# Performance work log

Measured on AMD Instinct MI355X. Metric: run time of the kernel, lower is better.

The kernel has to match this reference:

```python
import jax, jax.numpy as jnp
import numpy as np

DIM = 256
HALF = DIM // 2
B, S = 32, 4096
U_MAX = 4096          # upper bound on number of unique tree positions (positions < S)
MAX_DEPTH = 13        # bitlen(S) covers all path lengths for positions <= S


def setup_inputs() -> dict:
    key = jax.random.key(0)
    k1, k2, k3, k4, k5 = jax.random.split(key, 5)
    token_types = jax.random.randint(k1, (B, S), 0, 5, dtype=jnp.int32)
    node_positions = jax.random.randint(k2, (B, S), 0, S, dtype=jnp.int32)
    small_vals = jax.random.randint(k3, (B, S), 0, 4, dtype=jnp.int32)
    # deBruijn tokens (type 4) reference tree positions -> values must lie in unique(node_positions)
    token_values = jnp.where(token_types == 4, node_positions,
                   jnp.where(token_types == 3, -1, small_vals)).astype(jnp.int32)
    primitives = jax.random.normal(k4, (2, HALF, HALF), dtype=jnp.float32)
    identity = jnp.ones((1, HALF), dtype=jnp.float32)
    embed_weight = jax.random.normal(k5, (11, HALF), dtype=jnp.float32)
    return {"token_types": token_types, "token_values": token_values,
            "node_positions": node_positions, "primitives": primitives,
            "identity": identity, "embed_weight": embed_weight}


def cayley(X):
    # torch orthogonal(..., orthogonal_map='cayley'): A = tril(X) - tril(X)^T (skew), Q = (I - A/2)^{-1}(I + A/2)
    A = jnp.tril(X)
    A = A - jnp.swapaxes(A, -1, -2)
    I = jnp.eye(X.shape[-1], dtype=X.dtype)
    return jnp.linalg.solve(I - 0.5 * A, I + 0.5 * A)


def _forward(token_types, token_values, node_positions, primitives, identity, embed_weight):
    Q = cayley(primitives)                                   # [2, h, h] orthogonal maps
    flat_pos = node_positions.ravel()
    uniq, inv = jnp.unique(flat_pos, return_inverse=True, size=U_MAX, fill_value=S)
    inv = inv.ravel()

    # binary path of pos: bit d of pos for d < bitlen(pos)-1, padded with 2 (pos<=1 -> empty path)
    d = jnp.arange(MAX_DEPTH, dtype=uniq.dtype)
    bits = (uniq[:, None] >> d) & 1                           # [U, D]
    valid = (uniq[:, None] >> (d + 1)) > 0
    word = jnp.where(valid, bits, 2)                          # [U, D]

    maps0 = jnp.broadcast_to(identity, (U_MAX, HALF)).astype(primitives.dtype)

    def step(maps, b):                                        # maps [U, h], b [U]
        m0 = maps @ Q[0].T                                    # linear(maps, primitives[0])
        m1 = maps @ Q[1].T
        maps = jnp.where((b == 0)[:, None], m0,
                jnp.where((b == 1)[:, None], m1, maps))
        return maps, None

    path_emb, _ = jax.lax.scan(step, maps0, word.T)           # [U, h]

    pos_enc = path_emb[inv].reshape(B, S, HALF)               # positional encodings

    sos = token_types == 0
    bop = token_types == 1
    nop = token_types == 2
    oos = (token_types == 3) & (token_values == -1)
    db = token_types == 4

    emb_idx = jnp.where(bop, token_values + 1,
              jnp.where(nop, token_values + 5, 0))
    type_emb = embed_weight[emb_idx]                          # [B, S, h]

    db_idx = jnp.searchsorted(uniq, jnp.clip(token_values, 0, S - 1))  # bucketize into unique positions
    db_emb = path_emb[db_idx]                                 # [B, S, h]

    content = jnp.zeros_like(pos_enc)
    content = jnp.where(sos[..., None], embed_weight[0], content)
    content = jnp.where((bop | nop)[..., None], type_emb, content)
    content = jnp.where(db[..., None], db_emb, content)
    content = jnp.where(oos[..., None], embed_weight[10], content)

    return jnp.concatenate([content, pos_enc], axis=-1)       # [B, S, DIM]


def reference(token_types, token_values, node_positions, primitives, identity, embed_weight):
    return _forward(token_types, token_values, node_positions, primitives, identity, embed_weight)
```

## Files before the change

### kernel.cpp

```cpp
#include <hip/hip_runtime.h>

#define HALF 128
#define NMAT 16384
#define NTOK 131072

typedef float f4 __attribute__((ext_vector_type(4)));

__device__ __forceinline__ float nval(const float* __restrict__ X, int r, int c) {
    int mx = r > c ? r : c;
    int mn = r ^ c ^ mx;
    float x = X[mx * HALF + mn];
    return (r == c) ? 1.0f : (r > c ? 0.5f * x : -0.5f * x);
}

template<bool FIRST, bool LAST>
__global__ __launch_bounds__(256) void k1_step(const float* __restrict__ prim,
                                               const float* __restrict__ Win,
                                               float* __restrict__ Wout,
                                               int S) {
    __shared__ __align__(16) float Rs[16][132];
    __shared__ float Dc[16][17];
    __shared__ __align__(16) float RBs[16][132];
    __shared__ float Cs[16][17];

    const int blk = blockIdx.x;
    const int b   = blk >> 3;
    const int rg  = blk & 7;
    const int r0  = rg << 4;
    const int t   = threadIdx.x;
    const int k0  = S << 4;
    const float* __restrict__ X  = prim + b * NMAT;
    const float* __restrict__ Wi = Win  + b * NMAT;
    float*       __restrict__ Wo = Wout + b * NMAT;

    {
        const int j  = t >> 4;
        const int c0 = (t & 15) << 3;
        if (FIRST) {
            #pragma unroll
            for (int u = 0; u < 8; ++u) Rs[j][c0 + u] = nval(X, k0 + j, c0 + u);
        } else {
            float4 a  = *(const float4*)&Wi[(k0 + j) * HALF + c0];
            float4 b2 = *(const float4*)&Wi[(k0 + j) * HALF + c0 + 4];
            *(float4*)&Rs[j][c0]     = a;
            *(float4*)&Rs[j][c0 + 4] = b2;
        }
    }
    {
        const int rr = t >> 4, m = t & 15;
        Cs[rr][m] = FIRST ? nval(X, r0 + rr, k0 + m)
                          : Wi[(r0 + rr) * HALF + k0 + m];
    }
    __syncthreads();

    if (t < 64) {
        const int cp = t & 15, q4 = t >> 4;
        float dd[4];
        #pragma unroll
        for (int i = 0; i < 4; ++i) dd[i] = Rs[q4 * 4 + i][k0 + cp];
        #pragma unroll
        for (int k = 0; k < 16; ++k) {
            float cv[4];
            #pragma unroll
            for (int i = 0; i < 4; ++i) cv[i] = __shfl(dd[i], (q4 << 4) | k);
            float rv   = __shfl(dd[k & 3], ((k >> 2) << 4) | cp);
            float dkk  = __shfl(rv, k);
            float dinv = 1.0f / dkk;
            float sv   = rv * dinv;
            bool  own  = (cp == k);
            float rf   = own ? dinv : sv;
            #pragma unroll
            for (int i = 0; i < 4; ++i)
                dd[i] = own ? (-dd[i] * dinv) : fmaf(-cv[i], sv, dd[i]);
            dd[k & 3] = (q4 == (k >> 2)) ? rf : dd[k & 3];
        }
        #pragma unroll
        for (int i = 0; i < 4; ++i) Dc[cp][q4 * 4 + i] = dd[i];
    }
    __syncthreads();

    {
        const int m  = t >> 4;
        const int c0 = (t & 15) << 3;
        if (c0 == k0 || c0 == k0 + 8) {
            #pragma unroll
            for (int u = 0; u < 8; ++u) RBs[m][c0 + u] = Dc[c0 + u - k0][m];
        } else {
            float acc[8] = {0.f,0.f,0.f,0.f,0.f,0.f,0.f,0.f};
            #pragma unroll
            for (int j = 0; j < 16; ++j) {
                float dj = Dc[j][m];
                #pragma unroll
                for (int u = 0; u < 8; ++u)
                    acc[u] = fmaf(dj, Rs[j][c0 + u], acc[u]);
            }
            *(float4*)&RBs[m][c0]     = make_float4(acc[0], acc[1], acc[2], acc[3]);
            *(float4*)&RBs[m][c0 + 4] = make_float4(acc[4], acc[5], acc[6], acc[7]);
        }
    }
    __syncthreads();

    {
        const int rr = t >> 4;
        const int r  = r0 + rr;
        const int c0 = (t & 15) << 3;
        float w[8];

        if (rg == S) {
            #pragma unroll
            for (int u = 0; u < 8; ++u) w[u] = RBs[rr][c0 + u];
        } else {
            const bool pan = (c0 == k0) || (c0 == k0 + 8);
            if (pan) {
                #pragma unroll
                for (int u = 0; u < 8; ++u) w[u] = 0.0f;
            } else if (FIRST) {
                #pragma unroll
                for (int u = 0; u < 8; ++u) w[u] = nval(X, r, c0 + u);
            } else {
                float4 a  = *(const float4*)&Wi[r * HALF + c0];
                float4 b2 = *(const float4*)&Wi[r * HALF + c0 + 4];
                w[0]=a.x; w[1]=a.y; w[2]=a.z; w[3]=a.w;
                w[4]=b2.x; w[5]=b2.y; w[6]=b2.z; w[7]=b2.w;
            }
            #pragma unroll
            for (int m = 0; m < 16; ++m) {
                float cm = Cs[rr][m];
                #pragma unroll
                for (int u = 0; u < 8; ++u)
                    w[u] = fmaf(-cm, RBs[m][c0 + u], w[u]);
            }
        }

        if (LAST) {
            #pragma unroll
            for (int u = 0; u < 8; ++u)
                w[u] = 2.0f * w[u] - ((r == c0 + u) ? 1.0f : 0.0f);
        }
        *(float4*)&Wo[r * HALF + c0]     = make_float4(w[0], w[1], w[2], w[3]);
        *(float4*)&Wo[r * HALF + c0 + 4] = make_float4(w[4], w[5], w[6], w[7]);
    }
}

__global__ __launch_bounds__(256) void path_base(const float* __restrict__ QT,
                                                 const float* __restrict__ ident,
                                                 float* __restrict__ P) {
    __shared__ __align__(16) float vs[2][4][HALF];
    const int t    = threadIdx.x;
    const int rg   = t >> 6;
    const int jj   = (t & 63) << 1;
    const int v    = (blockIdx.x << 2) + rg;
    const int vmax = (blockIdx.x << 2) + 3;

    float2 cv = *(const float2*)&ident[jj];
    *(float2*)&vs[0][rg][jj] = cv;
    __syncthreads();

    int cur = 0;
    for (int d = 0; d < 8; ++d) {
        if ((vmax >> (d + 1)) == 0) break;
        const bool valid = (v >> (d + 1)) > 0;
        const float* __restrict__ Qm = QT + (((v >> d) & 1) ? NMAT : 0);
        float2 acc = make_float2(0.f, 0.f);
        #pragma unroll 4
        for (int cc = 0; cc < 128; cc += 4) {
            float4 v4 = *(const float4*)&vs[cur][rg][cc];
            float2 q0 = *(const float2*)&Qm[(cc+0)*HALF + jj];
            float2 q1 = *(const float2*)&Qm[(cc+1)*HALF + jj];
            float2 q2 = *(const float2*)&Qm[(cc+2)*HALF + jj];
            float2 q3 = *(const float2*)&Qm[(cc+3)*HALF + jj];
            acc.x = fmaf(v4.x,q0.x, fmaf(v4.y,q1.x, fmaf(v4.z,q2.x, fmaf(v4.w,q3.x, acc.x))));
            acc.y = fmaf(v4.x,q0.y, fmaf(v4.y,q1.y, fmaf(v4.z,q2.y, fmaf(v4.w,q3.y, acc.y))));
        }
        if (valid) cv = acc;
        *(float2*)&vs[cur ^ 1][rg][jj] = cv;
        __syncthreads();
        cur ^= 1;
    }
    *(float2*)&P[v * HALF + jj] = cv;
}

__global__ __launch_bounds__(256) void path_upper(const float* __restrict__ QT,
                                                  float* __restrict__ P) {
    __shared__ __align__(16) float vs[2][8][HALF];
    const int t  = threadIdx.x;
    const int j  = t & 127;
    const int h  = t >> 7;
    const int k  = 2 + (blockIdx.x >> 4);
    const int r0 = (blockIdx.x & 15) << 3;

    float acc[4];
    #pragma unroll
    for (int rr = 0; rr < 4; ++rr)
        acc[rr] = P[(128 + r0 + h * 4 + rr) * HALF + j];

    int p = 0;
    for (int d = 7; d < 13; ++d) {
        if ((k >> (d - 6)) == 0) break;
        const float* __restrict__ Qm = QT + (((k >> (d - 7)) & 1) ? NMAT : 0);
        #pragma unroll
        for (int rr = 0; rr < 4; ++rr) vs[p][h * 4 + rr][j] = acc[rr];
        __syncthreads();

        float nacc[4] = {0.f, 0.f, 0.f, 0.f};
        #pragma unroll 4
        for (int cc = 0; cc < 128; cc += 4) {
            float q0 = Qm[(cc + 0) * HALF + j];
            float q1 = Qm[(cc + 1) * HALF + j];
            float q2 = Qm[(cc + 2) * HALF + j];
            float q3 = Qm[(cc + 3) * HALF + j];
            #pragma unroll
            for (int rr = 0; rr < 4; ++rr) {
                float4 v4 = *(const float4*)&vs[p][h * 4 + rr][cc];
                nacc[rr] = fmaf(v4.x, q0,
                           fmaf(v4.y, q1,
                           fmaf(v4.z, q2,
                           fmaf(v4.w, q3, nacc[rr]))));
            }
        }
        #pragma unroll
        for (int rr = 0; rr < 4; ++rr) acc[rr] = nacc[rr];
        p ^= 1;
    }

    #pragma unroll
    for (int rr = 0; rr < 4; ++rr)
        P[((k << 7) | (r0 + h * 4 + rr)) * HALF + j] = acc[rr];
}

__global__ __launch_bounds__(256) void emit_out(const int* __restrict__ tt,
                                                const int* __restrict__ tv,
                                                const int* __restrict__ np,
                                                const float* __restrict__ P,
                                                const float* __restrict__ emb,
                                                float* __restrict__ out) {
    const int i  = (blockIdx.x << 2) + (threadIdx.x >> 6);
    const int jj = (threadIdx.x & 63) << 2;
    const int ty = tt[i];
    const int v  = tv[i];
    f4 val;
    if (jj < 128) {
        if (ty == 0)      val = *(const f4*)&emb[jj];
        else if (ty == 1) val = *(const f4*)&emb[(v + 1) * HALF + jj];
        else if (ty == 2) val = *(const f4*)&emb[(v + 5) * HALF + jj];
        else if (ty == 4) {
            int vc = v < 0 ? 0 : (v > 4095 ? 4095 : v);
            val = *(const f4*)&P[vc * HALF + jj];
        } else if (v == -1) val = *(const f4*)&emb[10 * HALF + jj];
        else { f4 z = {0.f, 0.f, 0.f, 0.f}; val = z; }
    } else {
        const int p = np[i];
        val = *(const f4*)&P[p * HALF + (jj - 128)];
    }
    __builtin_nontemporal_store(val, (f4*)&out[i * 256 + jj]);
}

extern "C" void kernel_launch(void* const* d_in, const int* in_sizes, int n_in,
                              void* d_out, int out_size, void* d_ws, size_t ws_size,
                              hipStream_t stream) {
    const int*   token_types = (const int*)  d_in[0];
    const int*   token_vals  = (const int*)  d_in[1];
    const int*   node_pos    = (const int*)  d_in[2];
    const float* prim        = (const float*)d_in[3];
    const float* ident       = (const float*)d_in[4];
    const float* emb         = (const float*)d_in[5];
    float* out = (float*)d_out;

    float* QT = (float*)d_ws;
    float* P  = (float*)((char*)d_ws + 262144);
    float* W0 = (float*)((char*)d_ws + 262144);
    float* W1 = (float*)((char*)d_ws + 262144 + 131072);

    k1_step<true,  false><<<16, 256, 0, stream>>>(prim, W0, W0, 0);
    k1_step<false, false><<<16, 256, 0, stream>>>(prim, W0, W1, 1);
    k1_step<false, false><<<16, 256, 0, stream>>>(prim, W1, W0, 2);
    k1_step<false, false><<<16, 256, 0, stream>>>(prim, W0, W1, 3);
    k1_step<false, false><<<16, 256, 0, stream>>>(prim, W1, W0, 4);
    k1_step<false, false><<<16, 256, 0, stream>>>(prim, W0, W1, 5);
    k1_step<false, false><<<16, 256, 0, stream>>>(prim, W1, W0, 6);
    k1_step<false, true ><<<16, 256, 0, stream>>>(prim, W0, QT, 7);

    path_base  <<<64,  256, 0, stream>>>(QT, ident, P);
    path_upper <<<480, 256, 0, stream>>>(QT, P);
    emit_out   <<<NTOK / 4, 256, 0, stream>>>(token_types, token_vals, node_pos,
                                              P, emb, out);
}
```

Before: 266.5 us.

## Fuse pairs of block Gauss-Jordan steps into one kernel launch

Merges two consecutive 16-column block elimination steps of the Cayley solve into a single kernel, halving the launches from eight to four. Each block also loads the next pivot panel and updates it locally in shared memory, so no global round-trip or grid-wide sync is needed between the paired steps. This cuts per-launch overhead and global traffic on a latency-bound chain of tiny kernels. In exchange it uses more shared memory and redoes some second-panel work redundantly in every block.

```diff
diff --git a/kernel.cpp b/kernel.cpp
--- a/kernel.cpp
+++ b/kernel.cpp
@@ -13,22 +13,98 @@
     return (r == c) ? 1.0f : (r > c ? 0.5f * x : -0.5f * x);
 }
 
-template<bool FIRST, bool LAST>
-__global__ __launch_bounds__(256) void k1_step(const float* __restrict__ prim,
-                                               const float* __restrict__ Win,
-                                               float* __restrict__ Wout,
-                                               int S) {
-    __shared__ __align__(16) float Rs[16][132];
-    __shared__ float Dc[16][17];
-    __shared__ __align__(16) float RBs[16][132];
-    __shared__ float Cs[16][17];
-
+__device__ __forceinline__ void gj16(const float (*Rs)[132], int kcol,
+                                     float (*Dc)[17], int t) {
+    const int cp = t & 15, q4 = t >> 4;
+    float dd[4];
+    #pragma unroll
+    for (int i = 0; i < 4; ++i) dd[i] = Rs[q4 * 4 + i][kcol + cp];
+    #pragma unroll
+    for (int k = 0; k < 16; ++k) {
+        float cv[4];
+        #pragma unroll
+        for (int i = 0; i < 4; ++i) cv[i] = __shfl(dd[i], (q4 << 4) | k);
+        float rv   = __shfl(dd[k & 3], ((k >> 2) << 4) | cp);
+        float dkk  = __shfl(rv, k);
+        float dinv = 1.0f / dkk;
+        float sv   = rv * dinv;
+        bool  own  = (cp == k);
+        float rf   = own ? dinv : sv;
+        #pragma unroll
+        for (int i = 0; i < 4; ++i)
+            dd[i] = own ? (-dd[i] * dinv) : fmaf(-cv[i], sv, dd[i]);
+        dd[k & 3] = (q4 == (k >> 2)) ? rf : dd[k & 3];
+    }
+    #pragma unroll
+    for (int i = 0; i < 4; ++i) Dc[cp][q4 * 4 + i] = dd[i];
+}
+
+__device__ __forceinline__ void rb_build(float (*RB)[132], const float (*Rs)[132],
+                                         const float (*Dc)[17], int kcol, int t) {
+    const int m  = t >> 4;
+    const int c0 = (t & 15) << 3;
+    if (c0 == kcol || c0 == kcol + 8) {
+        #pragma unroll
+        for (int u = 0; u < 8; ++u) RB[m][c0 + u] = Dc[c0 + u - kcol][m];
+    } else {
+        float acc[8] = {0.f,0.f,0.f,0.f,0.f,0.f,0.f,0.f};
+        #pragma unroll
+        for (int j = 0; j < 16; ++j) {
+            float dj = Dc[j][m];
+            #pragma unroll
+            for (int u = 0; u < 8; ++u)
+                acc[u] = fmaf(dj, Rs[j][c0 + u], acc[u]);
+        }
+        *(float4*)&RB[m][c0]     = make_float4(acc[0], acc[1], acc[2], acc[3]);
+        *(float4*)&RB[m][c0 + 4] = make_float4(acc[4], acc[5], acc[6], acc[7]);
+    }
+}
+
+__device__ __forceinline__ void adv(float (*A)[132], const float (*Cm)[17],
+                                    const float (*RB)[132], int kcol, int t) {
+    const int j  = t >> 4;
+    const int c0 = (t & 15) << 3;
+    const bool pan = (c0 == kcol) || (c0 == kcol + 8);
+    float w[8];
+    if (pan) {
+        #pragma unroll
+        for (int u = 0; u < 8; ++u) w[u] = 0.0f;
+    } else {
+        #pragma unroll
+        for (int u = 0; u < 8; ++u) w[u] = A[j][c0 + u];
+    }
+    #pragma unroll
+    for (int m = 0; m < 16; ++m) {
+        float cm = Cm[j][m];
+        #pragma unroll
+        for (int u = 0; u < 8; ++u)
+            w[u] = fmaf(-cm, RB[m][c0 + u], w[u]);
+    }
+    #pragma unroll
+    for (int u = 0; u < 8; ++u) A[j][c0 + u] = w[u];
+}
+
+template<int S0, bool FIRST, bool LAST>
+__global__ __launch_bounds__(256) void k1_2step(const float* __restrict__ prim,
+                                                const float* __restrict__ Win,
+                                                float* __restrict__ Wout) {
+    __shared__ __align__(16) float R1[16][132];
+    __shared__ __align__(16) float R2[16][132];
+    __shared__ __align__(16) float RB1[16][132];
+    __shared__ __align__(16) float RB2[16][132];
+    __shared__ __align__(16) float Wt[16][132];
+    __shared__ float Dc1[16][17];
+    __shared__ float Dc2[16][17];
+    __shared__ float C1[16][17];
+    __shared__ float C2[16][17];
+
+    constexpr int k0 = S0 << 4;
+    constexpr int k1 = (S0 + 1) << 4;
     const int blk = blockIdx.x;
     const int b   = blk >> 3;
     const int rg  = blk & 7;
     const int r0  = rg << 4;
     const int t   = threadIdx.x;
-    const int k0  = S << 4;
     const float* __restrict__ X  = prim + b * NMAT;
     const float* __restrict__ Wi = Win  + b * NMAT;
     float*       __restrict__ Wo = Wout + b * NMAT;
@@ -38,66 +114,47 @@
         const int c0 = (t & 15) << 3;
         if (FIRST) {
             #pragma unroll
-            for (int u = 0; u < 8; ++u) Rs[j][c0 + u] = nval(X, k0 + j, c0 + u);
+            for (int u = 0; u < 8; ++u) {
+                R1[j][c0 + u] = nval(X, k0 + j, c0 + u);
+                R2[j][c0 + u] = nval(X, k1 + j, c0 + u);
+                Wt[j][c0 + u] = nval(X, r0 + j, c0 + u);
+            }
+            C1[j][t & 15] = nval(X, r0 + j, k0 + (t & 15));
+            C2[j][t & 15] = nval(X, k1 + j, k0 + (t & 15));
         } else {
-            float4 a  = *(const float4*)&Wi[(k0 + j) * HALF + c0];
-            float4 b2 = *(const float4*)&Wi[(k0 + j) * HALF + c0 + 4];
-            *(float4*)&Rs[j][c0]     = a;
-            *(float4*)&Rs[j][c0 + 4] = b2;
-        }
-    }
+            *(float4*)&R1[j][c0]     = *(const float4*)&Wi[(k0 + j) * HALF + c0];
+            *(float4*)&R1[j][c0 + 4] = *(const float4*)&Wi[(k0 + j) * HALF + c0 + 4];
+            *(float4*)&R2[j][c0]     = *(const float4*)&Wi[(k1 + j) * HALF + c0];
+            *(float4*)&R2[j][c0 + 4] = *(const float4*)&Wi[(k1 + j) * HALF + c0 + 4];
+            *(float4*)&Wt[j][c0]     = *(const float4*)&Wi[(r0 + j) * HALF + c0];
+            *(float4*)&Wt[j][c0 + 4] = *(const float4*)&Wi[(r0 + j) * HALF + c0 + 4];
+            C1[j][t & 15] = Wi[(r0 + j) * HALF + k0 + (t & 15)];
+            C2[j][t & 15] = Wi[(k1 + j) * HALF + k0 + (t & 15)];
+        }
+    }
+    __syncthreads();
+
+    if (t < 64) gj16(R1, k0, Dc1, t);
+    __syncthreads();
+    rb_build(RB1, R1, Dc1, k0, t);
+    __syncthreads();
+
     {
-        const int rr = t >> 4, m = t & 15;
-        Cs[rr][m] = FIRST ? nval(X, r0 + rr, k0 + m)
-                          : Wi[(r0 + rr) * HALF + k0 + m];
-    }
-    __syncthreads();
-
-    if (t < 64) {
-        const int cp = t & 15, q4 = t >> 4;
-        float dd[4];
-        #pragma unroll
-        for (int i = 0; i < 4; ++i) dd[i] = Rs[q4 * 4 + i][k0 + cp];
-        #pragma unroll
-        for (int k = 0; k < 16; ++k) {
-            float cv[4];
-            #pragma unroll
-            for (int i = 0; i < 4; ++i) cv[i] = __shfl(dd[i], (q4 << 4) | k);
-            float rv   = __shfl(dd[k & 3], ((k >> 2) << 4) | cp);
-            float dkk  = __shfl(rv, k);
-            float dinv = 1.0f / dkk;
-            float sv   = rv * dinv;
-            bool  own  = (cp == k);
-            float rf   = own ? dinv : sv;
-            #pragma unroll
-            for (int i = 0; i < 4; ++i)
-                dd[i] = own ? (-dd[i] * dinv) : fmaf(-cv[i], sv, dd[i]);
-            dd[k & 3] = (q4 == (k >> 2)) ? rf : dd[k & 3];
-        }
-        #pragma unroll
-        for (int i = 0; i < 4; ++i) Dc[cp][q4 * 4 + i] = dd[i];
-    }
-    __syncthreads();
-
-    {
-        const int m  = t >> 4;
+        const int j  = t >> 4;
         const int c0 = (t & 15) << 3;
-        if (c0 == k0 || c0 == k0 + 8) {
-            #pragma unroll
-            for (int u = 0; u < 8; ++u) RBs[m][c0 + u] = Dc[c0 + u - k0][m];
+        if (rg == S0) {
+            #pragma unroll
+            for (int u = 0; u < 8; ++u) Wt[j][c0 + u] = RB1[j][c0 + u];
         } else {
-            float acc[8] = {0.f,0.f,0.f,0.f,0.f,0.f,0.f,0.f};
-            #pragma unroll
-            for (int j = 0; j < 16; ++j) {
-                float dj = Dc[j][m];
-                #pragma unroll
-                for (int u = 0; u < 8; ++u)
-                    acc[u] = fmaf(dj, Rs[j][c0 + u], acc[u]);
-            }
-            *(float4*)&RBs[m][c0]     = make_float4(acc[0], acc[1], acc[2], acc[3]);
-            *(float4*)&RBs[m][c0 + 4] = make_float4(acc[4], acc[5], acc[6], acc[7]);
-        }
-    }
+            adv(Wt, C1, RB1, k0, t);
+        }
+        adv(R2, C2, RB1, k0, t);
+    }
+    __syncthreads();
+
+    if (t < 64) gj16(R2, k1, Dc2, t);
+    __syncthreads();
+    rb_build(RB2, R2, Dc2, k1, t);
     __syncthreads();
 
     {
@@ -105,33 +162,26 @@
         const int r  = r0 + rr;
         const int c0 = (t & 15) << 3;
         float w[8];
-
-        if (rg == S) {
-            #pragma unroll
-            for (int u = 0; u < 8; ++u) w[u] = RBs[rr][c0 + u];
+        if (rg == S0 + 1) {
+            #pragma unroll
+            for (int u = 0; u < 8; ++u) w[u] = RB2[rr][c0 + u];
         } else {
-            const bool pan = (c0 == k0) || (c0 == k0 + 8);
+            const bool pan = (c0 == k1) || (c0 == k1 + 8);
             if (pan) {
                 #pragma unroll
                 for (int u = 0; u < 8; ++u) w[u] = 0.0f;
-            } else if (FIRST) {
+            } else {
                 #pragma unroll
-                for (int u = 0; u < 8; ++u) w[u] = nval(X, r, c0 + u);
-            } else {
-                float4 a  = *(const float4*)&Wi[r * HALF + c0];
-                float4 b2 = *(const float4*)&Wi[r * HALF + c0 + 4];
-                w[0]=a.x; w[1]=a.y; w[2]=a.z; w[3]=a.w;
-                w[4]=b2.x; w[5]=b2.y; w[6]=b2.z; w[7]=b2.w;
+                for (int u = 0; u < 8; ++u) w[u] = Wt[rr][c0 + u];
             }
             #pragma unroll
             for (int m = 0; m < 16; ++m) {
-                float cm = Cs[rr][m];
+                float cm = Wt[rr][k1 + m];
                 #pragma unroll
                 for (int u = 0; u < 8; ++u)
-                    w[u] = fmaf(-cm, RBs[m][c0 + u], w[u]);
+                    w[u] = fmaf(-cm, RB2[m][c0 + u], w[u]);
             }
         }
-
         if (LAST) {
             #pragma unroll
             for (int u = 0; u < 8; ++u)
@@ -271,14 +321,10 @@
     float* W0 = (float*)((char*)d_ws + 262144);
     float* W1 = (float*)((char*)d_ws + 262144 + 131072);
 
-    k1_step<true,  false><<<16, 256, 0, stream>>>(prim, W0, W0, 0);
-    k1_step<false, false><<<16, 256, 0, stream>>>(prim, W0, W1, 1);
-    k1_step<false, false><<<16, 256, 0, stream>>>(prim, W1, W0, 2);
-    k1_step<false, false><<<16, 256, 0, stream>>>(prim, W0, W1, 3);
-    k1_step<false, false><<<16, 256, 0, stream>>>(prim, W1, W0, 4);
-    k1_step<false, false><<<16, 256, 0, stream>>>(prim, W0, W1, 5);
-    k1_step<false, false><<<16, 256, 0, stream>>>(prim, W1, W0, 6);
-    k1_step<false, true ><<<16, 256, 0, stream>>>(prim, W0, QT, 7);
+    k1_2step<0, true,  false><<<16, 256, 0, stream>>>(prim, W0, W0);
+    k1_2step<2, false, false><<<16, 256, 0, stream>>>(prim, W0, W1);
+    k1_2step<4, false, false><<<16, 256, 0, stream>>>(prim, W1, W0);
+    k1_2step<6, false, true ><<<16, 256, 0, stream>>>(prim, W0, QT);
 
     path_base  <<<64,  256, 0, stream>>>(QT, ident, P);
     path_upper <<<480, 256, 0, stream>>>(QT, P);
```

Result: no change. 271.1 us (+1.7%).

## Merge eight Cayley elimination step launches into one persistent kernel with grid barrier

Applied to the files above, without the earlier changes.

Replaces eight sequential k1_step launches with a single persistent kernel that loops over the eight block-elimination steps. A software grid barrier (atomic counter in workspace, reset by a memset) separates the steps. The goal is to remove per-launch overhead and inter-kernel gaps in the small 16-block Cayley solve. In exchange it adds a memset, atomic spin-waits, and a dependence on all 16 blocks being co-resident.

```diff
diff --git a/kernel.cpp b/kernel.cpp
--- a/kernel.cpp
+++ b/kernel.cpp
@@ -13,11 +13,22 @@
     return (r == c) ? 1.0f : (r > c ? 0.5f * x : -0.5f * x);
 }
 
-template<bool FIRST, bool LAST>
-__global__ __launch_bounds__(256) void k1_step(const float* __restrict__ prim,
-                                               const float* __restrict__ Win,
-                                               float* __restrict__ Wout,
-                                               int S) {
+__device__ __forceinline__ void gbarrier(int* __restrict__ bar, int target, int t) {
+    __threadfence();
+    __syncthreads();
+    if (t == 0) {
+        atomicAdd(bar, 1);
+        while (atomicAdd(bar, 0) < target) __builtin_amdgcn_s_sleep(2);
+    }
+    __syncthreads();
+    __threadfence();
+}
+
+__global__ __launch_bounds__(256) void k1_persist(const float* __restrict__ prim,
+                                                  float* __restrict__ W0,
+                                                  float* __restrict__ W1,
+                                                  float* __restrict__ QT,
+                                                  int* __restrict__ bar) {
     __shared__ __align__(16) float Rs[16][132];
     __shared__ float Dc[16][17];
     __shared__ __align__(16) float RBs[16][132];
@@ -28,117 +39,126 @@
     const int rg  = blk & 7;
     const int r0  = rg << 4;
     const int t   = threadIdx.x;
-    const int k0  = S << 4;
-    const float* __restrict__ X  = prim + b * NMAT;
-    const float* __restrict__ Wi = Win  + b * NMAT;
-    float*       __restrict__ Wo = Wout + b * NMAT;
-
-    {
-        const int j  = t >> 4;
-        const int c0 = (t & 15) << 3;
-        if (FIRST) {
+    const float* __restrict__ X = prim + b * NMAT;
+
+    for (int S = 0; S < 8; ++S) {
+        const bool FIRST = (S == 0);
+        const bool LAST  = (S == 7);
+        const int  k0    = S << 4;
+        const float* __restrict__ Wi =
+            (FIRST ? W0 : (((S - 1) & 1) ? W1 : W0)) + b * NMAT;
+        float* __restrict__ Wo =
+            (LAST ? QT : ((S & 1) ? W1 : W0)) + b * NMAT;
+
+        {
+            const int j  = t >> 4;
+            const int c0 = (t & 15) << 3;
+            if (FIRST) {
+                #pragma unroll
+                for (int u = 0; u < 8; ++u) Rs[j][c0 + u] = nval(X, k0 + j, c0 + u);
+            } else {
+                float4 a  = *(const float4*)&Wi[(k0 + j) * HALF + c0];
+                float4 b2 = *(const float4*)&Wi[(k0 + j) * HALF + c0 + 4];
+                *(float4*)&Rs[j][c0]     = a;
+                *(float4*)&Rs[j][c0 + 4] = b2;
+            }
+        }
+        {
+            const int rr = t >> 4, m = t & 15;
+            Cs[rr][m] = FIRST ? nval(X, r0 + rr, k0 + m)
+                              : Wi[(r0 + rr) * HALF + k0 + m];
+        }
+        __syncthreads();
+
+        if (t < 64) {
+            const int cp = t & 15, q4 = t >> 4;
+            float dd[4];
             #pragma unroll
-            for (int u = 0; u < 8; ++u) Rs[j][c0 + u] = nval(X, k0 + j, c0 + u);
-        } else {
-            float4 a  = *(const float4*)&Wi[(k0 + j) * HALF + c0];
-            float4 b2 = *(const float4*)&Wi[(k0 + j) * HALF + c0 + 4];
-            *(float4*)&Rs[j][c0]     = a;
-            *(float4*)&Rs[j][c0 + 4] = b2;
-        }
-    }
-    {
-        const int rr = t >> 4, m = t & 15;
-        Cs[rr][m] = FIRST ? nval(X, r0 + rr, k0 + m)
-                          : Wi[(r0 + rr) * HALF + k0 + m];
-    }
-    __syncthreads();
-
-    if (t < 64) {
-        const int cp = t & 15, q4 = t >> 4;
-        float dd[4];
-        #pragma unroll
-        for (int i = 0; i < 4; ++i) dd[i] = Rs[q4 * 4 + i][k0 + cp];
-        #pragma unroll
-        for (int k = 0; k < 16; ++k) {
-            float cv[4];
+            for (int i = 0; i < 4; ++i) dd[i] = Rs[q4 * 4 + i][k0 + cp];
             #pragma unroll
-            for (int i = 0; i < 4; ++i) cv[i] = __shfl(dd[i], (q4 << 4) | k);
-            float rv   = __shfl(dd[k & 3], ((k >> 2) << 4) | cp);
-            float dkk  = __shfl(rv, k);
-            float dinv = 1.0f / dkk;
-            float sv   = rv * dinv;
-            bool  own  = (cp == k);
-            float rf   = own ? dinv : sv;
+            for (int k = 0; k < 16; ++k) {
+                float cv[4];
+                #pragma unroll
+                for (int i = 0; i < 4; ++i) cv[i] = __shfl(dd[i], (q4 << 4) | k);
+                float rv   = __shfl(dd[k & 3], ((k >> 2) << 4) | cp);
+                float dkk  = __shfl(rv, k);
+                float dinv = 1.0f / dkk;
+                float sv   = rv * dinv;
+                bool  own  = (cp == k);
+                float rf   = own ? dinv : sv;
+                #pragma unroll
+                for (int i = 0; i < 4; ++i)
+                    dd[i] = own ? (-dd[i] * dinv) : fmaf(-cv[i], sv, dd[i]);
+                dd[k & 3] = (q4 == (k >> 2)) ? rf : dd[k & 3];
+            }
             #pragma unroll
-            for (int i = 0; i < 4; ++i)
-                dd[i] = own ? (-dd[i] * dinv) : fmaf(-cv[i], sv, dd[i]);
-            dd[k & 3] = (q4 == (k >> 2)) ? rf : dd[k & 3];
-        }
-        #pragma unroll
-        for (int i = 0; i < 4; ++i) Dc[cp][q4 * 4 + i] = dd[i];
-    }
-    __syncthreads();
-
-    {
-        const int m  = t >> 4;
-        const int c0 = (t & 15) << 3;
-        if (c0 == k0 || c0 == k0 + 8) {
-            #pragma unroll
-            for (int u = 0; u < 8; ++u) RBs[m][c0 + u] = Dc[c0 + u - k0][m];
-        } else {
-            float acc[8] = {0.f,0.f,0.f,0.f,0.f,0.f,0.f,0.f};
-            #pragma unroll
-            for (int j = 0; j < 16; ++j) {
-                float dj = Dc[j][m];
+            for (int i = 0; i < 4; ++i) Dc[cp][q4 * 4 + i] = dd[i];
+        }
+        __syncthreads();
+
+        {
+            const int m  = t >> 4;
+            const int c0 = (t & 15) << 3;
+            if (c0 == k0 || c0 == k0 + 8) {
+                #pragma unroll
+                for (int u = 0; u < 8; ++u) RBs[m][c0 + u] = Dc[c0 + u - k0][m];
+            } else {
+                float acc[8] = {0.f,0.f,0.f,0.f,0.f,0.f,0.f,0.f};
+                #pragma unroll
+                for (int j = 0; j < 16; ++j) {
+                    float dj = Dc[j][m];
+                    #pragma unroll
+                    for (int u = 0; u < 8; ++u)
+                        acc[u] = fmaf(dj, Rs[j][c0 + u], acc[u]);
+                }
+                *(float4*)&RBs[m][c0]     = make_float4(acc[0], acc[1], acc[2], acc[3]);
+                *(float4*)&RBs[m][c0 + 4] = make_float4(acc[4], acc[5], acc[6], acc[7]);
+            }
+        }
+        __syncthreads();
+
+        {
+            const int rr = t >> 4;
+            const int r  = r0 + rr;
+            const int c0 = (t & 15) << 3;
+            float w[8];
+
+            if (rg == S) {
+                #pragma unroll
+                for (int u = 0; u < 8; ++u) w[u] = RBs[rr][c0 + u];
+            } else {
+                const bool pan = (c0 == k0) || (c0 == k0 + 8);
+                if (pan) {
+                    #pragma unroll
+                    for (int u = 0; u < 8; ++u) w[u] = 0.0f;
+                } else if (FIRST) {
+                    #pragma unroll
+                    for (int u = 0; u < 8; ++u) w[u] = nval(X, r, c0 + u);
+                } else {
+                    float4 a  = *(const float4*)&Wi[r * HALF + c0];
+                    float4 b2 = *(const float4*)&Wi[r * HALF + c0 + 4];
+                    w[0]=a.x; w[1]=a.y; w[2]=a.z; w[3]=a.w;
+                    w[4]=b2.x; w[5]=b2.y; w[6]=b2.z; w[7]=b2.w;
+                }
+                #pragma unroll
+                for (int m = 0; m < 16; ++m) {
+                    float cm = Cs[rr][m];
+                    #pragma unroll
+                    for (int u = 0; u < 8; ++u)
+                        w[u] = fmaf(-cm, RBs[m][c0 + u], w[u]);
+                }
+            }
+
+            if (LAST) {
                 #pragma unroll
                 for (int u = 0; u < 8; ++u)
-                    acc[u] = fmaf(dj, Rs[j][c0 + u], acc[u]);
-            }
-            *(float4*)&RBs[m][c0]     = make_float4(acc[0], acc[1], acc[2], acc[3]);
-            *(float4*)&RBs[m][c0 + 4] = make_float4(acc[4], acc[5], acc[6], acc[7]);
-        }
-    }
-    __syncthreads();
-
-    {
-        const int rr = t >> 4;
-        const int r  = r0 + rr;
-        const int c0 = (t & 15) << 3;
-        float w[8];
-
-        if (rg == S) {
-            #pragma unroll
-            for (int u = 0; u < 8; ++u) w[u] = RBs[rr][c0 + u];
-        } else {
-            const bool pan = (c0 == k0) || (c0 == k0 + 8);
-            if (pan) {
-                #pragma unroll
-                for (int u = 0; u < 8; ++u) w[u] = 0.0f;
-            } else if (FIRST) {
-                #pragma unroll
-                for (int u = 0; u < 8; ++u) w[u] = nval(X, r, c0 + u);
-            } else {
-                float4 a  = *(const float4*)&Wi[r * HALF + c0];
-                float4 b2 = *(const float4*)&Wi[r * HALF + c0 + 4];
-                w[0]=a.x; w[1]=a.y; w[2]=a.z; w[3]=a.w;
-                w[4]=b2.x; w[5]=b2.y; w[6]=b2.z; w[7]=b2.w;
-            }
-            #pragma unroll
-            for (int m = 0; m < 16; ++m) {
-                float cm = Cs[rr][m];
-                #pragma unroll
-                for (int u = 0; u < 8; ++u)
-                    w[u] = fmaf(-cm, RBs[m][c0 + u], w[u]);
-            }
-        }
-
-        if (LAST) {
-            #pragma unroll
-            for (int u = 0; u < 8; ++u)
-                w[u] = 2.0f * w[u] - ((r == c0 + u) ? 1.0f : 0.0f);
-        }
-        *(float4*)&Wo[r * HALF + c0]     = make_float4(w[0], w[1], w[2], w[3]);
-        *(float4*)&Wo[r * HALF + c0 + 4] = make_float4(w[4], w[5], w[6], w[7]);
+                    w[u] = 2.0f * w[u] - ((r == c0 + u) ? 1.0f : 0.0f);
+            }
+            *(float4*)&Wo[r * HALF + c0]     = make_float4(w[0], w[1], w[2], w[3]);
+            *(float4*)&Wo[r * HALF + c0 + 4] = make_float4(w[4], w[5], w[6], w[7]);
+        }
+
+        if (!LAST) gbarrier(bar, 16 * (S + 1), t);
     }
 }
 
@@ -266,20 +286,14 @@
     const float* emb         = (const float*)d_in[5];
     float* out = (float*)d_out;
 
-    float* QT = (float*)d_ws;
-    float* P  = (float*)((char*)d_ws + 262144);
-    float* W0 = (float*)((char*)d_ws + 262144);
-    float* W1 = (float*)((char*)d_ws + 262144 + 131072);
-
-    k1_step<true,  false><<<16, 256, 0, stream>>>(prim, W0, W0, 0);
-    k1_step<false, false><<<16, 256, 0, stream>>>(prim, W0, W1, 1);
-    k1_step<false, false><<<16, 256, 0, stream>>>(prim, W1, W0, 2);
-    k1_step<false, false><<<16, 256, 0, stream>>>(prim, W0, W1, 3);
-    k1_step<false, false><<<16, 256, 0, stream>>>(prim, W1, W0, 4);
-    k1_step<false, false><<<16, 256, 0, stream>>>(prim, W0, W1, 5);
-    k1_step<false, false><<<16, 256, 0, stream>>>(prim, W1, W0, 6);
-    k1_step<false, true ><<<16, 256, 0, stream>>>(prim, W0, QT, 7);
-
+    float* QT  = (float*)d_ws;
+    float* P   = (float*)((char*)d_ws + 262144);
+    float* W0  = (float*)((char*)d_ws + 262144);
+    float* W1  = (float*)((char*)d_ws + 262144 + 131072);
+    int*   bar = (int*)  ((char*)d_ws + 2359296);
+
+    hipMemsetAsync(bar, 0, 64, stream);
+    k1_persist <<<16,  256, 0, stream>>>(prim, W0, W1, QT, bar);
     path_base  <<<64,  256, 0, stream>>>(QT, ident, P);
     path_upper <<<480, 256, 0, stream>>>(QT, P);
     emit_out   <<<NTOK / 4, 256, 0, stream>>>(token_types, token_vals, node_pos,
```

After: 285.3 us. +7.1%, slower.
